# Kernel optimization log

Hardware: AMD Instinct MI355X
Metric: run time of the kernel (lower is better)

## Reference

```python
import jax, jax.numpy as jnp
import numpy as np

HEADS = 16
KEY_SIZE = 64
SIZE_PER_HEAD = 64
OUT_DIM = HEADS * SIZE_PER_HEAD  # 1024
BIG = 1e10
B, LQ, LK = 2, 2048, 2048


def setup_inputs() -> dict:
    key = jax.random.key(0)
    ks = jax.random.split(key, 8)
    q = jax.random.normal(ks[0], (B, LQ, OUT_DIM), dtype=jnp.float32)
    k = jax.random.normal(ks[1], (B, LK, OUT_DIM), dtype=jnp.float32)
    v = jax.random.normal(ks[2], (B, LK, OUT_DIM), dtype=jnp.float32)
    v_mask = (jax.random.uniform(ks[3], (B, LK)) > 0.1).astype(jnp.float32)
    q_mask = (jax.random.uniform(ks[4], (B, LQ)) > 0.1).astype(jnp.float32)
    # bias-free Linear weights, torch layout [out_features, in_features]
    s = 1.0 / np.sqrt(OUT_DIM)
    Wq = jax.random.normal(ks[5], (HEADS * KEY_SIZE, OUT_DIM), dtype=jnp.float32) * s
    Wk = jax.random.normal(ks[6], (HEADS * KEY_SIZE, OUT_DIM), dtype=jnp.float32) * s
    Wv = jax.random.normal(ks[7], (OUT_DIM, OUT_DIM), dtype=jnp.float32) * s
    return {"q": q, "k": k, "v": v, "v_mask": v_mask, "q_mask": q_mask,
            "Wq": Wq, "Wk": Wk, "Wv": Wv}


def _attention(q, k, v, v_mask, q_mask, Wq, Wk, Wv):
    b, lq, _ = q.shape
    lk = k.shape[1]
    # projections (torch Linear: x @ W.T)
    qw = jnp.einsum('bld,ed->ble', q, Wq).reshape(b, lq, HEADS, KEY_SIZE)
    kw = jnp.einsum('bld,ed->ble', k, Wk).reshape(b, lk, HEADS, KEY_SIZE)
    vw = jnp.einsum('bld,ed->ble', v, Wv).reshape(b, lk, HEADS, SIZE_PER_HEAD)
    # scores [B, H, Lq, Lk]
    a = jnp.einsum('bqhd,bkhd->bhqk', qw, kw) / np.sqrt(KEY_SIZE).astype(np.float32)
    # additive key-padding mask: a - (1 - v_mask) * BIG, broadcast over H and Lq
    a = a - (1.0 - v_mask)[:, None, None, :] * BIG
    # mask_right=True branch: mask = (1 - triu(ones, diag=1)) * BIG, i.e. lower
    # triangle INCLUDING the diagonal is penalized (faithful to source quirk).
    causal = jnp.tril(jnp.ones((lq, lk), dtype=a.dtype)) * BIG  # [Lq, Lk]
    a = a - causal[None, None, :, :]
    a = jax.nn.softmax(a, axis=-1)
    # output [B, Lq, H*dv]
    o = jnp.einsum('bhqk,bkhd->bqhd', a, vw).reshape(b, lq, OUT_DIM)
    o = o * q_mask[:, :, None]
    return o


def reference(q, k, v, v_mask, q_mask, Wq, Wk, Wv):
    return _attention(q, k, v, v_mask, q_mask, Wq, Wk, Wv)
```

## Files before the change

### kernel.cpp

```cpp
#include <hip/hip_runtime.h>
#include <hip/hip_bf16.h>
#include <stdint.h>

#define B_    2
#define SEQ   2048
#define EMB   1024
#define BIGF  1e10f
#define LOG2E 1.4426950408889634f
#define BIG2F (1e10f * LOG2E)
#define C2    (0.125f * LOG2E)

typedef unsigned short u16;
typedef __attribute__((ext_vector_type(4))) u16      u16x4;
typedef __attribute__((ext_vector_type(8))) short    bf8;
typedef __attribute__((ext_vector_type(4))) float    f4;
typedef __attribute__((ext_vector_type(4))) float    fv4;

__device__ inline float bf2f(u16 u){ union{uint32_t i; float f;} v; v.i = ((uint32_t)u) << 16; return v.f; }
__device__ inline u16 f2bf(float f){ union{float f; uint32_t i;} v; v.f = f;
                                     uint32_t r = v.i + 0x7fffu + ((v.i >> 16) & 1u); return (u16)(r >> 16); }
__device__ inline float exp2_hw(float x){ float r; asm("v_exp_f32 %0, %1" : "=v"(r) : "v"(x)); return r; }

__device__ inline void gl_lds16(const void* g, void* l){
  __builtin_amdgcn_global_load_lds((const __attribute__((address_space(1))) uint32_t*)g,
                                   (__attribute__((address_space(3))) uint32_t*)l, 16, 0, 0);
}

struct CvtArgs { const float* src[6]; u16* dst[6]; int n[6]; };

__global__ __launch_bounds__(256) void cvt_bf16(CvtArgs a)
{
  const int seg = blockIdx.y;
  const float* __restrict__ s = a.src[seg];
  u16* __restrict__ d = a.dst[seg];
  const int n = a.n[seg];
  const int i = (blockIdx.x * 256 + threadIdx.x) * 8;
  if (i >= n) return;
  fv4 x0 = *(const fv4*)(s + i);
  fv4 x1 = *(const fv4*)(s + i + 4);
  union { bf8 v; u16 u[8]; } o;
#pragma unroll
  for (int j = 0; j < 4; j++) { o.u[j] = f2bf(x0[j]); o.u[4 + j] = f2bf(x1[j]); }
  *(bf8*)(d + i) = o.v;
}

__global__ __launch_bounds__(256) void proj_gemm(
    const u16* __restrict__ Xq, const u16* __restrict__ Xk, const u16* __restrict__ Xv,
    const u16* __restrict__ Wq, const u16* __restrict__ Wk, const u16* __restrict__ Wv,
    u16* __restrict__ QH, u16* __restrict__ KH, u16* __restrict__ VTB)
{
  __shared__ u16 smem[18432];
  const int z = blockIdx.z;
  const u16* X = (z == 0) ? Xq : ((z == 1) ? Xk : Xv);
  const u16* W = (z == 0) ? Wq : ((z == 1) ? Wk : Wv);

  const int tid  = threadIdx.x;
  const int lane = tid & 63;
  const int w    = tid >> 6;
  const int wm   = w >> 1, wn = w & 1;
  const int m0   = blockIdx.x * 128;
  const int n0   = blockIdx.y * 128;
  const int col  = lane & 15, quad = lane >> 4;
  const int sq8  = (quad ^ ((col >> 1) & 3)) * 8;

  const int srow = w * 16 + (lane >> 2);
  const int sc   = ((lane & 3) ^ ((lane >> 3) & 3)) * 8;
  const size_t gA0 = (size_t)(m0 + srow) * 1024 + sc;
  const size_t gA1 = (size_t)(m0 + 64 + srow) * 1024 + sc;
  const size_t gB0 = (size_t)(n0 + srow) * 1024 + sc;
  const size_t gB1 = (size_t)(n0 + 64 + srow) * 1024 + sc;
  const int ldst = w * 512 + lane * 8;

#define PSTAGE(nb, kn) do { \
    gl_lds16(X + gA0 + (kn), &(nb)[ldst]); \
    gl_lds16(X + gA1 + (kn), &(nb)[2048 + ldst]); \
    gl_lds16(W + gB0 + (kn), &(nb)[4096 + ldst]); \
    gl_lds16(W + gB1 + (kn), &(nb)[6144 + ldst]); \
  } while (0)

  const f4 zero = {0.f, 0.f, 0.f, 0.f};
  f4 acc[4][4];
#pragma unroll
  for (int i = 0; i < 4; i++)
#pragma unroll
    for (int j = 0; j < 4; j++) acc[i][j] = zero;

  PSTAGE(smem, 0);
  PSTAGE((smem + 8192), 32);

#pragma unroll 2
  for (int t = 0; t < 31; t++) {
    asm volatile("s_waitcnt vmcnt(4)" ::: "memory");
    __builtin_amdgcn_s_barrier();
    __builtin_amdgcn_sched_barrier(0);
    const u16* cA = smem + (t & 1) * 8192;
    const u16* cB = cA + 4096;
    bf8 a[4], b[4];
#pragma unroll
    for (int tt = 0; tt < 4; tt++) a[tt] = *(const bf8*)&cA[(wm * 64 + tt * 16 + col) * 32 + sq8];
#pragma unroll
    for (int tt = 0; tt < 4; tt++) b[tt] = *(const bf8*)&cB[(wn * 64 + tt * 16 + col) * 32 + sq8];
    asm volatile("s_waitcnt lgkmcnt(0)" ::: "memory");
    __builtin_amdgcn_sched_barrier(0);
    __builtin_amdgcn_s_barrier();
    if (t < 30) {
      u16* nb = smem + (t & 1) * 8192;
      PSTAGE(nb, (t + 2) * 32);
    }
    __builtin_amdgcn_s_setprio(1);
#pragma unroll
    for (int mt = 0; mt < 4; mt++)
#pragma unroll
      for (int nt = 0; nt < 4; nt++)
        acc[mt][nt] = __builtin_amdgcn_mfma_f32_16x16x32_bf16(a[mt], b[nt], acc[mt][nt], 0, 0, 0);
    __builtin_amdgcn_s_setprio(0);
  }
  {
    asm volatile("s_waitcnt vmcnt(0)" ::: "memory");
    __builtin_amdgcn_s_barrier();
    __builtin_amdgcn_sched_barrier(0);
    const u16* cA = smem + 8192;
    const u16* cB = cA + 4096;
    bf8 a[4], b[4];
#pragma unroll
    for (int tt = 0; tt < 4; tt++) a[tt] = *(const bf8*)&cA[(wm * 64 + tt * 16 + col) * 32 + sq8];
#pragma unroll
    for (int tt = 0; tt < 4; tt++) b[tt] = *(const bf8*)&cB[(wn * 64 + tt * 16 + col) * 32 + sq8];
    __builtin_amdgcn_s_setprio(1);
#pragma unroll
    for (int mt = 0; mt < 4; mt++)
#pragma unroll
      for (int nt = 0; nt < 4; nt++)
        acc[mt][nt] = __builtin_amdgcn_mfma_f32_16x16x32_bf16(a[mt], b[nt], acc[mt][nt], 0, 0, 0);
    __builtin_amdgcn_s_setprio(0);
  }
#undef PSTAGE

  __syncthreads();
  u16* ep = &smem[w * 4608];

  if (z == 2) {
#pragma unroll
    for (int mt = 0; mt < 4; mt++)
#pragma unroll
      for (int nt = 0; nt < 4; nt++) {
        u16x4 pk = { f2bf(acc[mt][nt][0]), f2bf(acc[mt][nt][1]),
                     f2bf(acc[mt][nt][2]), f2bf(acc[mt][nt][3]) };
        *(u16x4*)&ep[(nt * 16 + col) * 72 + mt * 16 + quad * 4] = pk;
      }
  } else {
#pragma unroll
    for (int mt = 0; mt < 4; mt++)
#pragma unroll
      for (int nt = 0; nt < 4; nt++)
#pragma unroll
        for (int r = 0; r < 4; r++)
          ep[(mt * 16 + quad * 4 + r) * 72 + nt * 16 + col] = f2bf(acc[mt][nt][r]);
  }

  const int bb = m0 >> 11;
  const int h  = (n0 >> 6) + wn;
  const int bh = bb * 16 + h;

  if (z == 0) {
    const int qbase = (m0 & 2047) + wm * 64;
    u16* dst = QH + ((size_t)bh * SEQ + qbase) * 64;
#pragma unroll
    for (int i = 0; i < 8; i++) {
      const int f  = i * 1024 + lane * 16;
      const int ml = i * 8 + (lane >> 3), nl = (lane & 7) * 8;
      *(bf8*)(dst + (f >> 1)) = *(const bf8*)&ep[ml * 72 + nl];
    }
  } else if (z == 1) {
    const int kt = (((m0 & 2047) >> 6) + wm);
    u16* dst = KH + (((size_t)bh * 32 + kt) << 12);
#pragma unroll
    for (int i = 0; i < 8; i++) {
      const int f   = i * 1024 + lane * 16;
      const int dh  = f >> 12;
      const int klc = (f >> 6) & 63;
      const int dlo = (lane & 3) * 8;
      const int fs  = f ^ (((klc >> 1) & 3) << 4);
      *(bf8*)(dst + (fs >> 1)) = *(const bf8*)&ep[klc * 72 + dh * 32 + dlo];
    }
  } else {
    const int kt = (((m0 & 2047) >> 6) + wm);
    u16* dst = VTB + (((size_t)bh * 32 + kt) << 12);
#pragma unroll
    for (int i = 0; i < 8; i++) {
      const int f   = i * 1024 + lane * 16;
      const int kk  = f >> 12;
      const int d   = (f >> 6) & 63;
      const int klo = (lane & 3) * 8;
      const int fs  = f ^ (((d >> 1) & 3) << 4);
      *(bf8*)(dst + (fs >> 1)) = *(const bf8*)&ep[d * 72 + kk * 32 + klo];
    }
  }
}

__global__ __launch_bounds__(256) void sumv(const u16* __restrict__ VTB,
                                            const float* __restrict__ vmask,
                                            float* __restrict__ fb)
{
  const int w = threadIdx.x >> 6, lane = threadIdx.x & 63;
  const int gw = blockIdx.x * 4 + w;
  const int b = gw >> 10, e = gw & 1023;
  const int h = e >> 6, d = e & 63;
  const int bh = b * 16 + h;
  const float* vm = vmask + b * SEQ;
  const int ksw = (lane & 31) ^ (((d >> 1) & 3) << 3);
  float s = 0.f, c = 0.f;
  for (int kt = 0; kt < 32; kt++) {
    const u16 val = VTB[(((size_t)bh * 32 + kt) << 12) + (lane >> 5) * 2048 + d * 32 + ksw];
    const float m = vm[kt * 64 + lane];
    s += m * bf2f(val); c += m;
  }
#pragma unroll
  for (int o = 1; o < 64; o <<= 1) { s += __shfl_xor(s, o); c += __shfl_xor(c, o); }
  if (lane == 0) fb[gw] = s / c;
}

__global__ __launch_bounds__(256) void attn(
    const u16* __restrict__ QH, const u16* __restrict__ KH, const u16* __restrict__ VTB,
    const float* __restrict__ vmask, const float* __restrict__ qmask,
    const float* __restrict__ fb, float* __restrict__ OUT)
{
  __shared__ float pen[SEQ];
  __shared__ u16   sK[2][4096];
  __shared__ u16   sV[2][4096];
  __shared__ u16   P[4 * 16 * 72];

  const int tid = threadIdx.x, lane = tid & 63, w = tid >> 6;
  const int i   = blockIdx.x;
  const int xcd = i & 7;
  const int j   = i >> 3;
  const int qx  = j >> 2;
  const int bh  = xcd + 8 * (j & 3);
  const int b = bh >> 4, h = bh & 15;
  const int col = lane & 15, quad = lane >> 4;
  const int sq8 = (quad ^ ((col >> 1) & 3)) * 8;
  const int wb = w * 16 * 72;

  for (int t = tid; t < SEQ; t += 256)
    pen[t] = (1.0f - vmask[b * SEQ + t]) * BIG2F;

  const u16* kbase = KH  + (((size_t)bh * 32) << 12);
  const u16* vbase = VTB + (((size_t)bh * 32) << 12);

  const int q0 = qx * 64;

  bf8 bQ[2];
#pragma unroll
  for (int dh = 0; dh < 2; dh++)
    bQ[dh] = *(const bf8*)&QH[((size_t)bh * SEQ + q0 + w * 16 + col) * 64 + dh * 32 + quad * 8];

  const f4 zero = {0.f, 0.f, 0.f, 0.f};
  f4 accO[4];
  float l_acc = 0.f;
#pragma unroll
  for (int t = 0; t < 4; t++) accO[t] = zero;

  {
    const size_t toff = ((size_t)qx << 12) + w * 1024 + lane * 8;
    gl_lds16(kbase + toff,       &sK[0][w * 1024]);
    gl_lds16(kbase + toff + 512, &sK[0][w * 1024 + 512]);
    gl_lds16(vbase + toff,       &sV[0][w * 1024]);
    gl_lds16(vbase + toff + 512, &sV[0][w * 1024 + 512]);
  }

  const int ntile = 32 - qx;
  for (int it = 0; it < ntile; it++) {
    __syncthreads();
    if (it + 1 < ntile) {
      const int nb = (it + 1) & 1;
      const size_t toff = ((size_t)(qx + it + 1) << 12) + w * 1024 + lane * 8;
      gl_lds16(kbase + toff,       &sK[nb][w * 1024]);
      gl_lds16(kbase + toff + 512, &sK[nb][w * 1024 + 512]);
      gl_lds16(vbase + toff,       &sV[nb][w * 1024]);
      gl_lds16(vbase + toff + 512, &sV[nb][w * 1024 + 512]);
    }
    const u16* cK = sK[it & 1];
    const u16* cV = sV[it & 1];
    const int k0 = (qx + it) * 64;

    f4 accS[4];
#pragma unroll
    for (int t = 0; t < 4; t++) accS[t] = zero;
    __builtin_amdgcn_s_setprio(1);
#pragma unroll
    for (int nt = 0; nt < 4; nt++)
#pragma unroll
      for (int dh = 0; dh < 2; dh++) {
        bf8 aK = *(const bf8*)&cK[dh * 2048 + (nt * 16 + col) * 32 + sq8];
        accS[nt] = __builtin_amdgcn_mfma_f32_16x16x32_bf16(aK, bQ[dh], accS[nt], 0, 0, 0);
      }
    __builtin_amdgcn_s_setprio(0);

    float p[4][4];
    fv4 pv[4];
#pragma unroll
    for (int nt = 0; nt < 4; nt++) pv[nt] = *(const fv4*)&pen[k0 + nt * 16 + quad * 4];
    if (it == 0) {
#pragma unroll
      for (int nt = 0; nt < 4; nt++)
#pragma unroll
        for (int r = 0; r < 4; r++) {
          float sv = fmaf(accS[nt][r], C2, -pv[nt][r]);
          if (nt * 16 + quad * 4 + r <= w * 16 + col) sv -= BIG2F;
          p[nt][r] = exp2_hw(sv);
        }
    } else {
#pragma unroll
      for (int nt = 0; nt < 4; nt++)
#pragma unroll
        for (int r = 0; r < 4; r++)
          p[nt][r] = exp2_hw(fmaf(accS[nt][r], C2, -pv[nt][r]));
    }
#pragma unroll
    for (int nt = 0; nt < 4; nt++)
      l_acc += (p[nt][0] + p[nt][1]) + (p[nt][2] + p[nt][3]);

#pragma unroll
    for (int nt = 0; nt < 4; nt++) {
      union { u16x4 v; u16 u[4]; } pk;
      union { __hip_bfloat162 h2; u16 u[2]; } c0, c1;
      float2 f01; f01.x = p[nt][0]; f01.y = p[nt][1];
      float2 f23; f23.x = p[nt][2]; f23.y = p[nt][3];
      c0.h2 = __float22bfloat162_rn(f01);
      c1.h2 = __float22bfloat162_rn(f23);
      pk.u[0] = c0.u[0]; pk.u[1] = c0.u[1]; pk.u[2] = c1.u[0]; pk.u[3] = c1.u[1];
      *(u16x4*)&P[wb + col * 72 + nt * 16 + quad * 4] = pk.v;
    }

    __builtin_amdgcn_s_setprio(1);
#pragma unroll
    for (int kk = 0; kk < 2; kk++) {
      bf8 bP = *(const bf8*)&P[wb + col * 72 + kk * 32 + quad * 8];
#pragma unroll
      for (int nt = 0; nt < 4; nt++) {
        bf8 aV = *(const bf8*)&cV[kk * 2048 + (nt * 16 + col) * 32 + sq8];
        accO[nt] = __builtin_amdgcn_mfma_f32_16x16x32_bf16(aV, bP, accO[nt], 0, 0, 0);
      }
    }
    __builtin_amdgcn_s_setprio(0);
  }

  float l = l_acc;
  l += __shfl_xor(l, 16); l += __shfl_xor(l, 32);
  const int q = q0 + w * 16 + col;
  const float qm = qmask[b * SEQ + q];
  float* op = OUT + (size_t)(b * SEQ + q) * EMB + h * 64;
  if (l == 0.0f) {
#pragma unroll
    for (int nt = 0; nt < 4; nt++) {
      fv4 f = *(const fv4*)&fb[b * 1024 + h * 64 + nt * 16 + quad * 4];
      f *= qm;
      *(fv4*)(op + nt * 16 + quad * 4) = f;
    }
  } else {
    const float s = qm / l;
#pragma unroll
    for (int nt = 0; nt < 4; nt++) {
      fv4 f = { accO[nt][0] * s, accO[nt][1] * s, accO[nt][2] * s, accO[nt][3] * s };
      *(fv4*)(op + nt * 16 + quad * 4) = f;
    }
  }
}

extern "C" void kernel_launch(void* const* d_in, const int* in_sizes, int n_in,
                              void* d_out, int out_size, void* d_ws, size_t ws_size,
                              hipStream_t stream)
{
  const float* q  = (const float*)d_in[0];
  const float* k  = (const float*)d_in[1];
  const float* v  = (const float*)d_in[2];
  const float* vm = (const float*)d_in[3];
  const float* qm = (const float*)d_in[4];
  const float* Wq = (const float*)d_in[5];
  const float* Wk = (const float*)d_in[6];
  const float* Wv = (const float*)d_in[7];
  float* out = (float*)d_out;

  const size_t NBIG = (size_t)B_ * SEQ * EMB;
  const size_t NW   = (size_t)EMB * EMB;

  u16* qb  = (u16*)d_ws;
  u16* kb  = qb  + NBIG;
  u16* vb  = kb  + NBIG;
  u16* Wqb = vb  + NBIG;
  u16* Wkb = Wqb + NW;
  u16* Wvb = Wkb + NW;
  u16* QH  = Wvb + NW;
  u16* KH  = QH  + NBIG;
  u16* VTB = KH  + NBIG;
  float* fb = (float*)(VTB + NBIG);

  CvtArgs ca;
  ca.src[0] = q;  ca.dst[0] = qb;  ca.n[0] = (int)NBIG;
  ca.src[1] = k;  ca.dst[1] = kb;  ca.n[1] = (int)NBIG;
  ca.src[2] = v;  ca.dst[2] = vb;  ca.n[2] = (int)NBIG;
  ca.src[3] = Wq; ca.dst[3] = Wqb; ca.n[3] = (int)NW;
  ca.src[4] = Wk; ca.dst[4] = Wkb; ca.n[4] = (int)NW;
  ca.src[5] = Wv; ca.dst[5] = Wvb; ca.n[5] = (int)NW;

  cvt_bf16<<<dim3((unsigned)(NBIG / 8 / 256), 6, 1), 256, 0, stream>>>(ca);
  proj_gemm<<<dim3(32, 8, 3), 256, 0, stream>>>(qb, kb, vb, Wqb, Wkb, Wvb, QH, KH, VTB);
  sumv<<<dim3(512, 1, 1), 256, 0, stream>>>(VTB, vm, fb);
  attn<<<dim3(1024, 1, 1), 256, 0, stream>>>(QH, KH, VTB, vm, qm, fb, out);
}
```

Measured before the change: 178.7 us.

## Triple-buffer projection GEMM and deepen attention K/V prefetch pipeline

The projection GEMM moves from a two-stage to a three-stage LDS ring buffer, issuing loads three k-steps ahead with explicit vmcnt waits and a manually unrolled loop. The attention kernel now prefetches two K/V tiles ahead, synchronises with explicit waitcnt and barriers instead of __syncthreads, and hoists the penalty load ahead of the QK MFMAs. The aim is to hide global-to-LDS latency behind MFMA work. In exchange the GEMM uses more shared memory, which may lower occupancy, and the hand-tuned counter waits must match the number of loads in flight.

```diff
diff --git a/kernel.cpp b/kernel.cpp
--- a/kernel.cpp
+++ b/kernel.cpp
@@ -49,7 +49,7 @@
     const u16* __restrict__ Wq, const u16* __restrict__ Wk, const u16* __restrict__ Wv,
     u16* __restrict__ QH, u16* __restrict__ KH, u16* __restrict__ VTB)
 {
-  __shared__ u16 smem[18432];
+  __shared__ u16 smem[24576];
   const int z = blockIdx.z;
   const u16* X = (z == 0) ? Xq : ((z == 1) ? Xk : Xv);
   const u16* W = (z == 0) ? Wq : ((z == 1) ? Wk : Wv);
@@ -87,53 +87,42 @@
 
   PSTAGE(smem, 0);
   PSTAGE((smem + 8192), 32);
-
-#pragma unroll 2
-  for (int t = 0; t < 31; t++) {
-    asm volatile("s_waitcnt vmcnt(4)" ::: "memory");
-    __builtin_amdgcn_s_barrier();
-    __builtin_amdgcn_sched_barrier(0);
-    const u16* cA = smem + (t & 1) * 8192;
-    const u16* cB = cA + 4096;
-    bf8 a[4], b[4];
-#pragma unroll
-    for (int tt = 0; tt < 4; tt++) a[tt] = *(const bf8*)&cA[(wm * 64 + tt * 16 + col) * 32 + sq8];
-#pragma unroll
-    for (int tt = 0; tt < 4; tt++) b[tt] = *(const bf8*)&cB[(wn * 64 + tt * 16 + col) * 32 + sq8];
-    asm volatile("s_waitcnt lgkmcnt(0)" ::: "memory");
-    __builtin_amdgcn_sched_barrier(0);
-    __builtin_amdgcn_s_barrier();
-    if (t < 30) {
-      u16* nb = smem + (t & 1) * 8192;
-      PSTAGE(nb, (t + 2) * 32);
-    }
-    __builtin_amdgcn_s_setprio(1);
-#pragma unroll
-    for (int mt = 0; mt < 4; mt++)
-#pragma unroll
-      for (int nt = 0; nt < 4; nt++)
-        acc[mt][nt] = __builtin_amdgcn_mfma_f32_16x16x32_bf16(a[mt], b[nt], acc[mt][nt], 0, 0, 0);
-    __builtin_amdgcn_s_setprio(0);
-  }
-  {
-    asm volatile("s_waitcnt vmcnt(0)" ::: "memory");
-    __builtin_amdgcn_s_barrier();
-    __builtin_amdgcn_sched_barrier(0);
-    const u16* cA = smem + 8192;
-    const u16* cB = cA + 4096;
-    bf8 a[4], b[4];
-#pragma unroll
-    for (int tt = 0; tt < 4; tt++) a[tt] = *(const bf8*)&cA[(wm * 64 + tt * 16 + col) * 32 + sq8];
-#pragma unroll
-    for (int tt = 0; tt < 4; tt++) b[tt] = *(const bf8*)&cB[(wn * 64 + tt * 16 + col) * 32 + sq8];
-    __builtin_amdgcn_s_setprio(1);
-#pragma unroll
-    for (int mt = 0; mt < 4; mt++)
-#pragma unroll
-      for (int nt = 0; nt < 4; nt++)
-        acc[mt][nt] = __builtin_amdgcn_mfma_f32_16x16x32_bf16(a[mt], b[nt], acc[mt][nt], 0, 0, 0);
-    __builtin_amdgcn_s_setprio(0);
-  }
+  PSTAGE((smem + 16384), 64);
+
+#define PBODY(T, BASE, DOSTAGE) do { \
+    __builtin_amdgcn_s_barrier(); \
+    __builtin_amdgcn_sched_barrier(0); \
+    const u16* cA_ = (BASE); \
+    const u16* cB_ = (BASE) + 4096; \
+    bf8 a_[4], b_[4]; \
+    _Pragma("unroll") \
+    for (int tt = 0; tt < 4; tt++) a_[tt] = *(const bf8*)&cA_[(wm * 64 + tt * 16 + col) * 32 + sq8]; \
+    _Pragma("unroll") \
+    for (int tt = 0; tt < 4; tt++) b_[tt] = *(const bf8*)&cB_[(wn * 64 + tt * 16 + col) * 32 + sq8]; \
+    asm volatile("s_waitcnt lgkmcnt(0)" ::: "memory"); \
+    __builtin_amdgcn_sched_barrier(0); \
+    __builtin_amdgcn_s_barrier(); \
+    if (DOSTAGE) { PSTAGE((BASE), ((T) + 3) * 32); } \
+    __builtin_amdgcn_s_setprio(1); \
+    _Pragma("unroll") \
+    for (int mt = 0; mt < 4; mt++) \
+      _Pragma("unroll") \
+      for (int nt = 0; nt < 4; nt++) \
+        acc[mt][nt] = __builtin_amdgcn_mfma_f32_16x16x32_bf16(a_[mt], b_[nt], acc[mt][nt], 0, 0, 0); \
+    __builtin_amdgcn_s_setprio(0); \
+  } while (0)
+
+  for (int t3 = 0; t3 < 27; t3 += 3) {
+    asm volatile("s_waitcnt vmcnt(8)" ::: "memory"); PBODY(t3 + 0, smem, 1);
+    asm volatile("s_waitcnt vmcnt(8)" ::: "memory"); PBODY(t3 + 1, (smem + 8192), 1);
+    asm volatile("s_waitcnt vmcnt(8)" ::: "memory"); PBODY(t3 + 2, (smem + 16384), 1);
+  }
+  asm volatile("s_waitcnt vmcnt(8)" ::: "memory"); PBODY(27, smem, 1);
+  asm volatile("s_waitcnt vmcnt(8)" ::: "memory"); PBODY(28, (smem + 8192), 1);
+  asm volatile("s_waitcnt vmcnt(8)" ::: "memory"); PBODY(29, (smem + 16384), 0);
+  asm volatile("s_waitcnt vmcnt(4)" ::: "memory"); PBODY(30, smem, 0);
+  asm volatile("s_waitcnt vmcnt(0)" ::: "memory"); PBODY(31, (smem + 8192), 0);
+#undef PBODY
 #undef PSTAGE
 
   __syncthreads();
@@ -260,28 +249,31 @@
 #pragma unroll
   for (int t = 0; t < 4; t++) accO[t] = zero;
 
-  {
-    const size_t toff = ((size_t)qx << 12) + w * 1024 + lane * 8;
-    gl_lds16(kbase + toff,       &sK[0][w * 1024]);
-    gl_lds16(kbase + toff + 512, &sK[0][w * 1024 + 512]);
-    gl_lds16(vbase + toff,       &sV[0][w * 1024]);
-    gl_lds16(vbase + toff + 512, &sV[0][w * 1024 + 512]);
-  }
+#define ASTAGE(BUF, KT) do { \
+    const size_t toff_ = ((size_t)(KT) << 12) + w * 1024 + lane * 8; \
+    gl_lds16(kbase + toff_,       &sK[(BUF)][w * 1024]); \
+    gl_lds16(kbase + toff_ + 512, &sK[(BUF)][w * 1024 + 512]); \
+    gl_lds16(vbase + toff_,       &sV[(BUF)][w * 1024]); \
+    gl_lds16(vbase + toff_ + 512, &sV[(BUF)][w * 1024 + 512]); \
+  } while (0)
 
   const int ntile = 32 - qx;
+  ASTAGE(0, qx);
+  ASTAGE(1, qx + 1);
+
   for (int it = 0; it < ntile; it++) {
-    __syncthreads();
-    if (it + 1 < ntile) {
-      const int nb = (it + 1) & 1;
-      const size_t toff = ((size_t)(qx + it + 1) << 12) + w * 1024 + lane * 8;
-      gl_lds16(kbase + toff,       &sK[nb][w * 1024]);
-      gl_lds16(kbase + toff + 512, &sK[nb][w * 1024 + 512]);
-      gl_lds16(vbase + toff,       &sV[nb][w * 1024]);
-      gl_lds16(vbase + toff + 512, &sV[nb][w * 1024 + 512]);
-    }
+    if (it + 1 < ntile) asm volatile("s_waitcnt vmcnt(4) lgkmcnt(0)" ::: "memory");
+    else                asm volatile("s_waitcnt vmcnt(0) lgkmcnt(0)" ::: "memory");
+    __builtin_amdgcn_s_barrier();
+    __builtin_amdgcn_sched_barrier(0);
+
     const u16* cK = sK[it & 1];
     const u16* cV = sV[it & 1];
     const int k0 = (qx + it) * 64;
+
+    fv4 pv[4];
+#pragma unroll
+    for (int nt = 0; nt < 4; nt++) pv[nt] = *(const fv4*)&pen[k0 + nt * 16 + quad * 4];
 
     f4 accS[4];
 #pragma unroll
@@ -297,9 +289,6 @@
     __builtin_amdgcn_s_setprio(0);
 
     float p[4][4];
-    fv4 pv[4];
-#pragma unroll
-    for (int nt = 0; nt < 4; nt++) pv[nt] = *(const fv4*)&pen[k0 + nt * 16 + quad * 4];
     if (it == 0) {
 #pragma unroll
       for (int nt = 0; nt < 4; nt++)
@@ -343,7 +332,13 @@
       }
     }
     __builtin_amdgcn_s_setprio(0);
-  }
+
+    asm volatile("s_waitcnt lgkmcnt(0)" ::: "memory");
+    __builtin_amdgcn_sched_barrier(0);
+    __builtin_amdgcn_s_barrier();
+    if (it + 2 < ntile) { ASTAGE((it & 1), qx + it + 2); }
+  }
+#undef ASTAGE
 
   float l = l_acc;
   l += __shfl_xor(l, 16); l += __shfl_xor(l, 32);
```

New measurement: 178.8 us (median of 2 runs). No clear change (+0.1%).
